# Kernel tuning notes

Measured on AMD Instinct MI355X. Metric: run time of the kernel, lower is better.

## Reference

```python
import jax, jax.numpy as jnp
import numpy as np

N_STATE = 1024
N_HEAD = 16
HEAD_DIM = N_STATE // N_HEAD
SEQLENS = [1024, 896, 768, 640, 512, 384, 896, 1024]  # sum = 6144
TOTAL = sum(SEQLENS)


def setup_inputs() -> dict:
    key = jax.random.key(0)
    ks = jax.random.split(key, 8)
    s = 0.02
    cu = jnp.asarray(np.concatenate([[0], np.cumsum(SEQLENS)]), dtype=jnp.int32)
    return {
        "x": jax.random.normal(ks[0], (TOTAL, N_STATE), jnp.float32),
        "cu_seqlens": cu,
        "Wq": jax.random.normal(ks[1], (N_STATE, N_STATE), jnp.float32) * s,
        "bq": jax.random.normal(ks[2], (N_STATE,), jnp.float32) * s,
        "Wk": jax.random.normal(ks[3], (N_STATE, N_STATE), jnp.float32) * s,
        "Wv": jax.random.normal(ks[4], (N_STATE, N_STATE), jnp.float32) * s,
        "bv": jax.random.normal(ks[5], (N_STATE,), jnp.float32) * s,
        "Wo": jax.random.normal(ks[6], (N_STATE, N_STATE), jnp.float32) * s,
        "bo": jax.random.normal(ks[7], (N_STATE,), jnp.float32) * s,
    }


def reference(x, cu_seqlens, Wq, bq, Wk, Wv, bv, Wo, bo):
    # cu_seqlens is a static (host) quantity in the original (used via .tolist())
    cu = np.asarray(jax.device_get(cu_seqlens))
    seqlens = cu[1:] - cu[:-1]
    B = len(seqlens)
    Lmax = int(seqlens.max())

    q = x @ Wq.T + bq              # [T, n_state]
    k = x @ Wk.T                   # key has no bias
    v = x @ Wv.T + bv

    # static pad/unpad index maps (honoring the ragged structure)
    ar = np.arange(Lmax)
    valid = ar[None, :] < seqlens[:, None]             # [B, Lmax]
    idx = np.where(valid, cu[:-1, None] + ar[None, :], 0)
    unpad_idx = np.nonzero(valid.reshape(-1))[0]       # flat positions of real tokens
    valid_j = jnp.asarray(valid)

    def pad(t):  # [T, n_state] -> [B, Lmax, H, D], zeros in padding
        p = jnp.where(valid_j[:, :, None], t[idx], 0.0)
        return p.reshape(B, Lmax, N_HEAD, HEAD_DIM)

    qp, kp, vp = pad(q), pad(k), pad(v)
    scale = HEAD_DIM ** -0.5
    # torch adds the bool mask (True->1.0) after masked_fill(mask==0, -max):
    # valid keys get +1.0 (softmax-invariant shift), invalid keys get -finfo.max
    big_neg = jnp.finfo(x.dtype).max
    add_mask = jnp.where(valid_j, 1.0, -big_neg)[:, None, None, :]  # [B,1,1,Lmax]

    scores = jnp.einsum("bqhd,bkhd->bhqk", qp, kp) * scale + add_mask
    weights = jax.nn.softmax(scores, axis=-1)
    ctx = jnp.einsum("bhqk,bkhd->bqhd", weights, vp)   # [B, Lmax, H, D]
    ctx_flat = ctx.reshape(B * Lmax, N_STATE)[unpad_idx]  # [T, n_state]
    return ctx_flat @ Wo.T + bo
```

## Files before the change

kernel.cpp:

```cpp
#include <hip/hip_runtime.h>

typedef unsigned short u16;
typedef unsigned int u32;
typedef __attribute__((ext_vector_type(8))) short bf16x8;
typedef __attribute__((ext_vector_type(4))) float f32x4;

#define MFMA_BF16(a, b, c) __builtin_amdgcn_mfma_f32_16x16x32_bf16((a), (b), (c), 0, 0, 0)

#define QSCALE 0.18033688011112042f

__device__ __forceinline__ u16 f2bf(float f) {
    union { float f; unsigned u; } v; v.f = f;
    return (u16)((v.u + 0x7FFFu + ((v.u >> 16) & 1u)) >> 16);
}

__device__ __forceinline__ u32 pkbf(float a, float b) {
    union { float f; unsigned u; } x, y; x.f = a; y.f = b;
    return ((x.u + 0x8000u) >> 16) | ((y.u + 0x8000u) & 0xFFFF0000u);
}

__device__ __forceinline__ void async16(const void* g, void* l) {
    __builtin_amdgcn_global_load_lds(
        (const __attribute__((address_space(1))) void*)g,
        (__attribute__((address_space(3))) void*)l, 16, 0, 0);
}

__global__ __launch_bounds__(256) void cvt_all(
    const float* __restrict__ x, const float* __restrict__ Wq, const float* __restrict__ Wk,
    const float* __restrict__ Wv, const float* __restrict__ Wo,
    u16* __restrict__ xb, u16* __restrict__ Wqb, u16* __restrict__ Wkb,
    u16* __restrict__ Wvb, u16* __restrict__ Wob) {
    int b = blockIdx.x;
    const float* src; u16* dst; int base;
    if (b < 6144)      { src = x;  dst = xb;  base = b; }
    else if (b < 7168) { src = Wq; dst = Wqb; base = b - 6144; }
    else if (b < 8192) { src = Wk; dst = Wkb; base = b - 7168; }
    else if (b < 9216) { src = Wv; dst = Wvb; base = b - 8192; }
    else               { src = Wo; dst = Wob; base = b - 9216; }
    int i = base * 256 + threadIdx.x;
    float4 v = ((const float4*)src)[i];
    unsigned long long pk = (unsigned long long)f2bf(v.x)
                          | ((unsigned long long)f2bf(v.y) << 16)
                          | ((unsigned long long)f2bf(v.z) << 32)
                          | ((unsigned long long)f2bf(v.w) << 48);
    *(unsigned long long*)(dst + (size_t)i * 4) = pk;
}

__global__ __launch_bounds__(256) void gemm_qkv(
    const u16* __restrict__ xb,
    const u16* __restrict__ Wqb, const u16* __restrict__ Wkb, const u16* __restrict__ Wvb,
    const float* __restrict__ bq, const float* __restrict__ bv,
    u16* __restrict__ qb, u16* __restrict__ kb, u16* __restrict__ vbT) {
    __shared__ __align__(16) u16 As[128 * 64];
    __shared__ __align__(16) u16 Bs[128 * 64];
    const int tid = threadIdx.x;

    const int fid = blockIdx.x;
    const int xcd = fid & 7;
    const int slot = fid >> 3;
    const int mloc = slot % 6;
    const int nidx = slot / 6;
    const int m0 = (xcd * 6 + mloc) << 7;
    const int buf = nidx >> 3;
    const int n0 = (nidx & 7) << 7;
    const u16* __restrict__ W = (buf == 0) ? Wqb : (buf == 1) ? Wkb : Wvb;

    const int rr = tid >> 3;
    const int cg = tid & 7;
    const int wv = tid >> 6, lane = tid & 63, g = lane >> 4, c = lane & 15;
    const int wm = (wv & 1) << 6, wn = (wv >> 1) << 6;

    const int sw = (cg ^ (rr & 7)) << 3;
    const u16* gA[4]; const u16* gB[4];
#pragma unroll
    for (int r = 0; r < 4; ++r) {
        gA[r] = xb + (size_t)(m0 + (r << 5) + rr) * 1024 + sw;
        gB[r] = W + (size_t)(n0 + (r << 5) + rr) * 1024 + sw;
    }

    f32x4 zero = {0.f, 0.f, 0.f, 0.f};
    f32x4 acc[4][4];
#pragma unroll
    for (int i = 0; i < 4; ++i)
#pragma unroll
        for (int j = 0; j < 4; ++j) acc[i][j] = zero;

    for (int kt = 0; kt < 16; ++kt) {
        const int k0 = kt << 6;
        __syncthreads();
#pragma unroll
        for (int r = 0; r < 4; ++r) {
            async16(gA[r] + k0, &As[(r << 11) + tid * 8]);
            async16(gB[r] + k0, &Bs[(r << 11) + tid * 8]);
        }
        __syncthreads();
#pragma unroll
        for (int ks = 0; ks < 2; ++ks) {
            bf16x8 af[4], bb[4];
#pragma unroll
            for (int i = 0; i < 4; ++i) {
                int ra = wm + (i << 4) + c;
                af[i] = *(const bf16x8*)(&As[ra * 64 + ((((ks << 2) + g) ^ (ra & 7)) << 3)]);
                int rb = wn + (i << 4) + c;
                bb[i] = *(const bf16x8*)(&Bs[rb * 64 + ((((ks << 2) + g) ^ (rb & 7)) << 3)]);
            }
#pragma unroll
            for (int i = 0; i < 4; ++i)
#pragma unroll
                for (int j = 0; j < 4; ++j) acc[i][j] = MFMA_BF16(af[i], bb[j], acc[i][j]);
        }
    }

    if (buf == 0) {
#pragma unroll
        for (int j = 0; j < 4; ++j) {
            int col = n0 + wn + (j << 4) + c;
            float bias = bq[col];
#pragma unroll
            for (int i = 0; i < 4; ++i) {
                int rowb = m0 + wm + (i << 4) + (g << 2);
#pragma unroll
                for (int r = 0; r < 4; ++r)
                    qb[(size_t)(rowb + r) * 1024 + col] = f2bf((acc[i][j][r] + bias) * QSCALE);
            }
        }
    } else if (buf == 1) {
#pragma unroll
        for (int j = 0; j < 4; ++j) {
            int col = n0 + wn + (j << 4) + c;
#pragma unroll
            for (int i = 0; i < 4; ++i) {
                int rowb = m0 + wm + (i << 4) + (g << 2);
#pragma unroll
                for (int r = 0; r < 4; ++r)
                    kb[(size_t)(rowb + r) * 1024 + col] = f2bf(acc[i][j][r]);
            }
        }
    } else {
#pragma unroll
        for (int j = 0; j < 4; ++j) {
            int col = n0 + wn + (j << 4) + c;
            float bias = bv[col];
#pragma unroll
            for (int i = 0; i < 4; ++i) {
                int trow = m0 + wm + (i << 4) + (g << 2);
                unsigned long long pk =
                      (unsigned long long)f2bf(acc[i][j][0] + bias)
                    | ((unsigned long long)f2bf(acc[i][j][1] + bias) << 16)
                    | ((unsigned long long)f2bf(acc[i][j][2] + bias) << 32)
                    | ((unsigned long long)f2bf(acc[i][j][3] + bias) << 48);
                *(unsigned long long*)(vbT + (size_t)col * 6144 + trow) = pk;
            }
        }
    }
}

__global__ __launch_bounds__(256) void gemm_out(
    const u16* __restrict__ ctxb, const u16* __restrict__ Wob,
    const float* __restrict__ bo, float* __restrict__ out) {
    __shared__ __align__(16) u16 As[64 * 64];
    __shared__ __align__(16) u16 Bs[64 * 64];
    const int tid = threadIdx.x;

    const int fid = blockIdx.x;
    const int xcd = fid & 7;
    const int slot = fid >> 3;
    const int mloc = slot % 12;
    const int nidx = slot / 12;
    const int m0 = (xcd * 12 + mloc) << 6;
    const int n0 = nidx << 6;

    const int rr = tid >> 3, cg = tid & 7;
    const int wv = tid >> 6, lane = tid & 63, g = lane >> 4, c = lane & 15;
    const int wm = (wv & 1) << 5, wn = (wv >> 1) << 5;

    const int sw = (cg ^ (rr & 7)) << 3;
    const u16* gA[2]; const u16* gB[2];
#pragma unroll
    for (int r = 0; r < 2; ++r) {
        gA[r] = ctxb + (size_t)(m0 + (r << 5) + rr) * 1024 + sw;
        gB[r] = Wob + (size_t)(n0 + (r << 5) + rr) * 1024 + sw;
    }

    f32x4 zero = {0.f, 0.f, 0.f, 0.f};
    f32x4 acc[2][2];
#pragma unroll
    for (int i = 0; i < 2; ++i)
#pragma unroll
        for (int j = 0; j < 2; ++j) acc[i][j] = zero;

    for (int kt = 0; kt < 16; ++kt) {
        const int k0 = kt << 6;
        __syncthreads();
#pragma unroll
        for (int r = 0; r < 2; ++r) {
            async16(gA[r] + k0, &As[(r << 11) + tid * 8]);
            async16(gB[r] + k0, &Bs[(r << 11) + tid * 8]);
        }
        __syncthreads();
#pragma unroll
        for (int ks = 0; ks < 2; ++ks) {
            bf16x8 af[2], bb[2];
#pragma unroll
            for (int i = 0; i < 2; ++i) {
                int ra = wm + (i << 4) + c;
                af[i] = *(const bf16x8*)(&As[ra * 64 + ((((ks << 2) + g) ^ (ra & 7)) << 3)]);
                int rb = wn + (i << 4) + c;
                bb[i] = *(const bf16x8*)(&Bs[rb * 64 + ((((ks << 2) + g) ^ (rb & 7)) << 3)]);
            }
#pragma unroll
            for (int i = 0; i < 2; ++i)
#pragma unroll
                for (int j = 0; j < 2; ++j) acc[i][j] = MFMA_BF16(af[i], bb[j], acc[i][j]);
        }
    }

#pragma unroll
    for (int j = 0; j < 2; ++j) {
        int col = n0 + wn + (j << 4) + c;
        float bias = bo[col];
#pragma unroll
        for (int i = 0; i < 2; ++i) {
            int rowb = m0 + wm + (i << 4) + (g << 2);
#pragma unroll
            for (int r = 0; r < 4; ++r)
                out[(size_t)(rowb + r) * 1024 + col] = acc[i][j][r] + bias;
        }
    }
}

__global__ __launch_bounds__(256) void attn_kernel(const u16* __restrict__ qb,
                                                   const u16* __restrict__ kb,
                                                   const u16* __restrict__ vbT,
                                                   u16* __restrict__ ctxb) {
    __shared__ __align__(16) u16 Ks[128 * 64];
    __shared__ __align__(16) u16 Vs[64 * 128];
    __shared__ __align__(16) u16 Ps[4 * 2048];

    const int tid = threadIdx.x;
    const int fid = blockIdx.x;
    const int xcd = fid & 7;
    const int slot = fid >> 3;
    const int h = (xcd << 1) + (slot >= 96 ? 1 : 0);
    const int q0 = (slot % 96) << 6;

    const int cuv[9] = {0, 1024, 1920, 2688, 3328, 3840, 4224, 5120, 6144};
    int s0 = 0, e0 = 6144;
#pragma unroll
    for (int i = 1; i < 8; ++i) {
        if (q0 >= cuv[i]) s0 = cuv[i];
        if (q0 < cuv[i] && cuv[i] < e0) e0 = cuv[i];
    }
    const int ntiles = (e0 - s0) >> 7;

    const int wv = tid >> 6, lane = tid & 63, g = lane >> 4, c = lane & 15;
    const int wrow = wv << 4;

    {
        const int rr = tid >> 3, cg = tid & 7;
#pragma unroll
        for (int r = 0; r < 2; ++r) {
            int row = (r << 5) + rr;
            async16(qb + (size_t)(q0 + row) * 1024 + (h << 6) + ((cg ^ (row & 7)) << 3),
                    Ps + (r << 11) + tid * 8);
        }
    }
    __syncthreads();

    bf16x8 qf[2];
#pragma unroll
    for (int ks = 0; ks < 2; ++ks) {
        int row = wrow + c;
        qf[ks] = *(const bf16x8*)(Ps + row * 64 + ((((ks << 2) + g) ^ (row & 7)) << 3));
    }

    float m_run = -1e30f, l_run = 0.f;
    f32x4 zero = {0.f, 0.f, 0.f, 0.f};
    f32x4 oacc[4];
#pragma unroll
    for (int nt = 0; nt < 4; ++nt) oacc[nt] = zero;

    const int pbase = (wv << 11) + c * 128;
    const int c7 = c & 7;

    for (int kt = 0; kt < ntiles; ++kt) {
        const int kv0 = s0 + (kt << 7);
        __syncthreads();
        {
            const int rr = tid >> 3, cg = tid & 7;
#pragma unroll
            for (int r = 0; r < 4; ++r) {
                int row = (r << 5) + rr;
                async16(kb + (size_t)(kv0 + row) * 1024 + (h << 6) + ((cg ^ (row & 7)) << 3),
                        Ks + (r << 11) + tid * 8);
            }
            const int rr2 = tid >> 4, cg2 = tid & 15;
#pragma unroll
            for (int r = 0; r < 4; ++r) {
                int row = (r << 4) + rr2;
                async16(vbT + (size_t)((h << 6) + row) * 6144 + kv0 + ((cg2 ^ (row & 15)) << 3),
                        Vs + (r << 11) + tid * 8);
            }
        }
        __syncthreads();

        f32x4 st[8];
#pragma unroll
        for (int mt = 0; mt < 8; ++mt) st[mt] = zero;
#pragma unroll
        for (int mt = 0; mt < 8; ++mt) {
            int row = (mt << 4) + c;
            int sw = row & 7;
#pragma unroll
            for (int ks = 0; ks < 2; ++ks) {
                bf16x8 kf = *(const bf16x8*)(&Ks[row * 64 + ((((ks << 2) + g) ^ sw) << 3)]);
                st[mt] = MFMA_BF16(kf, qf[ks], st[mt]);
            }
        }

        float mx = st[0][0];
#pragma unroll
        for (int mt = 0; mt < 8; ++mt)
#pragma unroll
            for (int r = 0; r < 4; ++r) mx = fmaxf(mx, st[mt][r]);
        mx = fmaxf(mx, __shfl_xor(mx, 16, 64));
        mx = fmaxf(mx, __shfl_xor(mx, 32, 64));
        float mnew = fmaxf(m_run, mx);
        float alpha = exp2f(m_run - mnew);
        m_run = mnew;

        float rsum = 0.f;
#pragma unroll
        for (int mt = 0; mt < 8; ++mt) {
            float p0 = exp2f(st[mt][0] - mnew);
            float p1 = exp2f(st[mt][1] - mnew);
            float p2 = exp2f(st[mt][2] - mnew);
            float p3 = exp2f(st[mt][3] - mnew);
            rsum += (p0 + p1) + (p2 + p3);
            int ph = ((mt << 2) + g) ^ (c7 << 1);
            *(uint2*)(Ps + pbase + (ph << 2)) = make_uint2(pkbf(p0, p1), pkbf(p2, p3));
        }
        rsum += __shfl_xor(rsum, 16, 64);
        rsum += __shfl_xor(rsum, 32, 64);
        l_run = l_run * alpha + rsum;

        float al[4];
#pragma unroll
        for (int r = 0; r < 4; ++r) al[r] = __shfl(alpha, (g << 2) + r, 16);
#pragma unroll
        for (int nt = 0; nt < 4; ++nt)
#pragma unroll
            for (int r = 0; r < 4; ++r) oacc[nt][r] *= al[r];

#pragma unroll
        for (int ks = 0; ks < 4; ++ks) {
            int pg = ((ks << 2) + g) ^ c7;
            bf16x8 pf = *(const bf16x8*)(Ps + pbase + (pg << 3));
#pragma unroll
            for (int nt = 0; nt < 4; ++nt) {
                int vrow = (nt << 4) + c;
                bf16x8 vf = *(const bf16x8*)(&Vs[vrow * 128 + ((((ks << 2) + g) ^ (vrow & 15)) << 3)]);
                oacc[nt] = MFMA_BF16(pf, vf, oacc[nt]);
            }
        }
    }

    float inv = 1.0f / l_run;
    float invr[4];
#pragma unroll
    for (int r = 0; r < 4; ++r) invr[r] = __shfl(inv, (g << 2) + r, 16);
#pragma unroll
    for (int r = 0; r < 4; ++r) {
        size_t rowoff = (size_t)(q0 + wrow + (g << 2) + r) * 1024 + (h << 6);
#pragma unroll
        for (int nt = 0; nt < 4; ++nt)
            ctxb[rowoff + (nt << 4) + c] = f2bf(oacc[nt][r] * invr[r]);
    }
}

extern "C" void kernel_launch(void* const* d_in, const int* in_sizes, int n_in,
                              void* d_out, int out_size, void* d_ws, size_t ws_size,
                              hipStream_t stream) {
    const float* x  = (const float*)d_in[0];
    const float* Wq = (const float*)d_in[2];
    const float* bq = (const float*)d_in[3];
    const float* Wk = (const float*)d_in[4];
    const float* Wv = (const float*)d_in[5];
    const float* bv = (const float*)d_in[6];
    const float* Wo = (const float*)d_in[7];
    const float* bo = (const float*)d_in[8];
    float* out = (float*)d_out;

    u16* ws = (u16*)d_ws;
    u16* xb   = ws;
    u16* Wqb  = xb + 6291456;
    u16* Wkb  = Wqb + 1048576;
    u16* Wvb  = Wkb + 1048576;
    u16* Wob  = Wvb + 1048576;
    u16* qb   = Wob + 1048576;
    u16* kb   = qb + 6291456;
    u16* vbT  = kb + 6291456;
    u16* ctxb = xb;

    cvt_all<<<10240, 256, 0, stream>>>(x, Wq, Wk, Wv, Wo, xb, Wqb, Wkb, Wvb, Wob);
    gemm_qkv<<<1152, 256, 0, stream>>>(xb, Wqb, Wkb, Wvb, bq, bv, qb, kb, vbT);
    attn_kernel<<<1536, 256, 0, stream>>>(qb, kb, vbT, ctxb);
    gemm_out<<<1536, 256, 0, stream>>>(ctxb, Wob, bo, out);
}
```

Baseline: 233.4 us.

## Double-buffer GEMM LDS tiles and transpose MFMA operands for vectorized epilogue stores

Both projection GEMMs now double-buffer their LDS tiles, prefetching the next K slice with async global-to-LDS loads while the current slice is consumed. This uses one barrier per iteration instead of two. The QKV GEMM shrinks its K step to 32 with a new swizzle, and for Q/K and the output GEMM it swaps the MFMA operands so each lane holds four consecutive output columns. That allows 8-byte packed bf16 stores and float4 output stores with vector bias loads. The risk is that relying on a single barrier with no explicit wait on the async loads could race, and the extra LDS may reduce occupancy.

```diff
diff --git a/kernel.cpp b/kernel.cpp
--- a/kernel.cpp
+++ b/kernel.cpp
@@ -51,8 +51,8 @@
     const u16* __restrict__ Wqb, const u16* __restrict__ Wkb, const u16* __restrict__ Wvb,
     const float* __restrict__ bq, const float* __restrict__ bv,
     u16* __restrict__ qb, u16* __restrict__ kb, u16* __restrict__ vbT) {
-    __shared__ __align__(16) u16 As[128 * 64];
-    __shared__ __align__(16) u16 Bs[128 * 64];
+    __shared__ __align__(16) u16 As[2][128 * 32];
+    __shared__ __align__(16) u16 Bs[2][128 * 32];
     const int tid = threadIdx.x;
 
     const int fid = blockIdx.x;
@@ -65,18 +65,16 @@
     const int n0 = (nidx & 7) << 7;
     const u16* __restrict__ W = (buf == 0) ? Wqb : (buf == 1) ? Wkb : Wvb;
 
-    const int rr = tid >> 3;
-    const int cg = tid & 7;
+    const int srow = tid >> 2;
+    const int scg = tid & 3;
     const int wv = tid >> 6, lane = tid & 63, g = lane >> 4, c = lane & 15;
     const int wm = (wv & 1) << 6, wn = (wv >> 1) << 6;
 
-    const int sw = (cg ^ (rr & 7)) << 3;
-    const u16* gA[4]; const u16* gB[4];
-#pragma unroll
-    for (int r = 0; r < 4; ++r) {
-        gA[r] = xb + (size_t)(m0 + (r << 5) + rr) * 1024 + sw;
-        gB[r] = W + (size_t)(n0 + (r << 5) + rr) * 1024 + sw;
-    }
+    const u16* gA0 = xb + (size_t)(m0 + srow) * 1024;
+    const u16* gA1 = xb + (size_t)(m0 + 64 + srow) * 1024;
+    const u16* gB0 = W + (size_t)(n0 + srow) * 1024;
+    const u16* gB1 = W + (size_t)(n0 + 64 + srow) * 1024;
+    const int sw0 = (scg ^ ((srow >> 1) & 3)) << 3;
 
     f32x4 zero = {0.f, 0.f, 0.f, 0.f};
     f32x4 acc[4][4];
@@ -85,55 +83,72 @@
 #pragma unroll
         for (int j = 0; j < 4; ++j) acc[i][j] = zero;
 
-    for (int kt = 0; kt < 16; ++kt) {
-        const int k0 = kt << 6;
+    async16(gA0 + sw0, &As[0][tid * 8]);
+    async16(gB0 + sw0, &Bs[0][tid * 8]);
+    async16(gA1 + sw0, &As[0][2048 + tid * 8]);
+    async16(gB1 + sw0, &Bs[0][2048 + tid * 8]);
+
+#pragma unroll 2
+    for (int kt = 0; kt < 32; ++kt) {
+        const int cur = kt & 1;
         __syncthreads();
-#pragma unroll
-        for (int r = 0; r < 4; ++r) {
-            async16(gA[r] + k0, &As[(r << 11) + tid * 8]);
-            async16(gB[r] + k0, &Bs[(r << 11) + tid * 8]);
-        }
-        __syncthreads();
-#pragma unroll
-        for (int ks = 0; ks < 2; ++ks) {
-            bf16x8 af[4], bb[4];
-#pragma unroll
-            for (int i = 0; i < 4; ++i) {
-                int ra = wm + (i << 4) + c;
-                af[i] = *(const bf16x8*)(&As[ra * 64 + ((((ks << 2) + g) ^ (ra & 7)) << 3)]);
-                int rb = wn + (i << 4) + c;
-                bb[i] = *(const bf16x8*)(&Bs[rb * 64 + ((((ks << 2) + g) ^ (rb & 7)) << 3)]);
-            }
+        if (kt < 31) {
+            const int gc = (kt + 1) << 5;
+            async16(gA0 + gc + sw0, &As[cur ^ 1][tid * 8]);
+            async16(gB0 + gc + sw0, &Bs[cur ^ 1][tid * 8]);
+            async16(gA1 + gc + sw0, &As[cur ^ 1][2048 + tid * 8]);
+            async16(gB1 + gc + sw0, &Bs[cur ^ 1][2048 + tid * 8]);
+        }
+        bf16x8 af[4], bb[4];
+#pragma unroll
+        for (int i = 0; i < 4; ++i) {
+            int ra = wm + (i << 4) + c;
+            af[i] = *(const bf16x8*)(&As[cur][ra * 32 + ((g ^ ((ra >> 1) & 3)) << 3)]);
+            int rb = wn + (i << 4) + c;
+            bb[i] = *(const bf16x8*)(&Bs[cur][rb * 32 + ((g ^ ((rb >> 1) & 3)) << 3)]);
+        }
+        if (buf < 2) {
 #pragma unroll
             for (int i = 0; i < 4; ++i)
 #pragma unroll
+                for (int j = 0; j < 4; ++j) acc[i][j] = MFMA_BF16(bb[j], af[i], acc[i][j]);
+        } else {
+#pragma unroll
+            for (int i = 0; i < 4; ++i)
+#pragma unroll
                 for (int j = 0; j < 4; ++j) acc[i][j] = MFMA_BF16(af[i], bb[j], acc[i][j]);
         }
     }
 
     if (buf == 0) {
 #pragma unroll
-        for (int j = 0; j < 4; ++j) {
-            int col = n0 + wn + (j << 4) + c;
-            float bias = bq[col];
-#pragma unroll
-            for (int i = 0; i < 4; ++i) {
-                int rowb = m0 + wm + (i << 4) + (g << 2);
-#pragma unroll
-                for (int r = 0; r < 4; ++r)
-                    qb[(size_t)(rowb + r) * 1024 + col] = f2bf((acc[i][j][r] + bias) * QSCALE);
+        for (int i = 0; i < 4; ++i) {
+            const size_t mrow = (size_t)(m0 + wm + (i << 4) + c) * 1024;
+#pragma unroll
+            for (int j = 0; j < 4; ++j) {
+                int ncol = n0 + wn + (j << 4) + (g << 2);
+                const float4 b4 = *(const float4*)(bq + ncol);
+                unsigned long long pk =
+                      (unsigned long long)f2bf((acc[i][j][0] + b4.x) * QSCALE)
+                    | ((unsigned long long)f2bf((acc[i][j][1] + b4.y) * QSCALE) << 16)
+                    | ((unsigned long long)f2bf((acc[i][j][2] + b4.z) * QSCALE) << 32)
+                    | ((unsigned long long)f2bf((acc[i][j][3] + b4.w) * QSCALE) << 48);
+                *(unsigned long long*)(qb + mrow + ncol) = pk;
             }
         }
     } else if (buf == 1) {
 #pragma unroll
-        for (int j = 0; j < 4; ++j) {
-            int col = n0 + wn + (j << 4) + c;
-#pragma unroll
-            for (int i = 0; i < 4; ++i) {
-                int rowb = m0 + wm + (i << 4) + (g << 2);
-#pragma unroll
-                for (int r = 0; r < 4; ++r)
-                    kb[(size_t)(rowb + r) * 1024 + col] = f2bf(acc[i][j][r]);
+        for (int i = 0; i < 4; ++i) {
+            const size_t mrow = (size_t)(m0 + wm + (i << 4) + c) * 1024;
+#pragma unroll
+            for (int j = 0; j < 4; ++j) {
+                int ncol = n0 + wn + (j << 4) + (g << 2);
+                unsigned long long pk =
+                      (unsigned long long)f2bf(acc[i][j][0])
+                    | ((unsigned long long)f2bf(acc[i][j][1]) << 16)
+                    | ((unsigned long long)f2bf(acc[i][j][2]) << 32)
+                    | ((unsigned long long)f2bf(acc[i][j][3]) << 48);
+                *(unsigned long long*)(kb + mrow + ncol) = pk;
             }
         }
     } else {
@@ -158,8 +173,8 @@
 __global__ __launch_bounds__(256) void gemm_out(
     const u16* __restrict__ ctxb, const u16* __restrict__ Wob,
     const float* __restrict__ bo, float* __restrict__ out) {
-    __shared__ __align__(16) u16 As[64 * 64];
-    __shared__ __align__(16) u16 Bs[64 * 64];
+    __shared__ __align__(16) u16 As[2][64 * 64];
+    __shared__ __align__(16) u16 Bs[2][64 * 64];
     const int tid = threadIdx.x;
 
     const int fid = blockIdx.x;
@@ -189,42 +204,54 @@
 #pragma unroll
         for (int j = 0; j < 2; ++j) acc[i][j] = zero;
 
+#pragma unroll
+    for (int r = 0; r < 2; ++r) {
+        async16(gA[r], &As[0][(r << 11) + tid * 8]);
+        async16(gB[r], &Bs[0][(r << 11) + tid * 8]);
+    }
+
+#pragma unroll 2
     for (int kt = 0; kt < 16; ++kt) {
-        const int k0 = kt << 6;
+        const int cur = kt & 1;
         __syncthreads();
-#pragma unroll
-        for (int r = 0; r < 2; ++r) {
-            async16(gA[r] + k0, &As[(r << 11) + tid * 8]);
-            async16(gB[r] + k0, &Bs[(r << 11) + tid * 8]);
-        }
-        __syncthreads();
+        if (kt < 15) {
+            const int gc = (kt + 1) << 6;
+#pragma unroll
+            for (int r = 0; r < 2; ++r) {
+                async16(gA[r] + gc, &As[cur ^ 1][(r << 11) + tid * 8]);
+                async16(gB[r] + gc, &Bs[cur ^ 1][(r << 11) + tid * 8]);
+            }
+        }
 #pragma unroll
         for (int ks = 0; ks < 2; ++ks) {
             bf16x8 af[2], bb[2];
 #pragma unroll
             for (int i = 0; i < 2; ++i) {
                 int ra = wm + (i << 4) + c;
-                af[i] = *(const bf16x8*)(&As[ra * 64 + ((((ks << 2) + g) ^ (ra & 7)) << 3)]);
+                af[i] = *(const bf16x8*)(&As[cur][ra * 64 + ((((ks << 2) + g) ^ (ra & 7)) << 3)]);
                 int rb = wn + (i << 4) + c;
-                bb[i] = *(const bf16x8*)(&Bs[rb * 64 + ((((ks << 2) + g) ^ (rb & 7)) << 3)]);
+                bb[i] = *(const bf16x8*)(&Bs[cur][rb * 64 + ((((ks << 2) + g) ^ (rb & 7)) << 3)]);
             }
 #pragma unroll
             for (int i = 0; i < 2; ++i)
 #pragma unroll
-                for (int j = 0; j < 2; ++j) acc[i][j] = MFMA_BF16(af[i], bb[j], acc[i][j]);
-        }
-    }
-
-#pragma unroll
-    for (int j = 0; j < 2; ++j) {
-        int col = n0 + wn + (j << 4) + c;
-        float bias = bo[col];
-#pragma unroll
-        for (int i = 0; i < 2; ++i) {
-            int rowb = m0 + wm + (i << 4) + (g << 2);
-#pragma unroll
-            for (int r = 0; r < 4; ++r)
-                out[(size_t)(rowb + r) * 1024 + col] = acc[i][j][r] + bias;
+                for (int j = 0; j < 2; ++j) acc[i][j] = MFMA_BF16(bb[j], af[i], acc[i][j]);
+        }
+    }
+
+#pragma unroll
+    for (int i = 0; i < 2; ++i) {
+        const size_t mrow = (size_t)(m0 + wm + (i << 4) + c) * 1024;
+#pragma unroll
+        for (int j = 0; j < 2; ++j) {
+            int ncol = n0 + wn + (j << 4) + (g << 2);
+            const float4 b4 = *(const float4*)(bo + ncol);
+            float4 o;
+            o.x = acc[i][j][0] + b4.x;
+            o.y = acc[i][j][1] + b4.y;
+            o.z = acc[i][j][2] + b4.z;
+            o.w = acc[i][j][3] + b4.w;
+            *(float4*)(out + mrow + ncol) = o;
         }
     }
 }
```

After: 271.2 us. 1.16x slower.
